# Optimization experiments

Hardware: AMD Instinct MI355X
Metric: run time of the kernel (lower is better)

The kernel has to match this reference:

```python
import math
import jax, jax.numpy as jnp
import numpy as np

D_MODEL, STATE_DIM, SEQ_L = 256, 64, 8192


def setup_inputs() -> dict:
    key = jax.random.key(0)
    ks = jax.random.split(key, 6)
    d, N = D_MODEL, STATE_DIM
    s = 1.0 / math.sqrt(N)
    return {
        "Lambda_re": jax.random.normal(ks[0], (d, N), jnp.float32),
        "Lambda_im": jax.random.normal(ks[1], (d, N), jnp.float32),
        "P_re": jax.random.normal(ks[2], (d, N), jnp.float32) * s,
        "P_im": jax.random.normal(ks[3], (d, N), jnp.float32) * s,
        "B_re": jax.random.normal(ks[4], (d, N), jnp.float32) * s,
        "B_im": jnp.zeros((d, N), jnp.float32),
        "log_dt": jax.random.uniform(ks[5], (d,), jnp.float32,
                                     math.log(1e-3), math.log(0.1)),
        "D": jnp.zeros((d,), jnpp := jnp.float32) if False else jnp.zeros((d,), jnp.float32),
        "L": SEQ_L,
    }


def reference(Lambda_re, Lambda_im, P_re, P_im, B_re, B_im, log_dt, D, L):
    # NPLR / Cauchy-Woodbury S4 kernel (learn_cd=False -> C = B, D is a zero buffer)
    Lam = (-jax.nn.softplus(Lambda_re) + 1j * Lambda_im).astype(jnp.complex64)  # [d, N]
    P = (P_re + 1j * P_im).astype(jnp.complex64)                                # [d, N]
    B = (B_re + 1j * B_im).astype(jnp.complex64)                                # [d, N]
    dt = jnp.exp(log_dt)                                                        # [d]

    k = jnp.arange(L)
    z = jnp.exp((-2j * jnp.pi / L) * k).astype(jnp.complex64)                   # [L] roots of unity
    eps = jnp.finfo(jnp.float32).eps
    denom_z = 1.0 + z
    denom_z = jnp.where(jnp.abs(denom_z) < eps, jnp.complex64(eps), denom_z)

    # Bilinear-transform frequencies g: [d, L] complex
    g = (2.0 / dt)[:, None] * ((1.0 - z) / denom_z)[None, :]

    # Cauchy resolvent R: [d, L, N] complex (the dominant intermediate)
    R = 1.0 / (g[:, :, None] - Lam[:, None, :])

    Pc, Bc = jnp.conj(P), jnp.conj(B)
    PRB = jnp.einsum('dn,dln,dn->dl', Pc, R, B)
    PRP = jnp.einsum('dn,dln,dn->dl', Pc, R, P)
    BRB = jnp.einsum('dn,dln,dn->dl', Bc, R, B)
    BRP = jnp.einsum('dn,dln,dn->dl', Bc, R, P)

    # Woodbury rank-1 correction, then undo the bilinear prefactor
    K_hat = (2.0 / denom_z)[None, :] * (BRB - BRP * PRB / (1.0 + PRP))          # [d, L]
    K = jnp.fft.ifft(K_hat, n=L, axis=-1).real.astype(jnp.float32)
    return (K, D)
```

## Files before the change

### kernel.cpp

```cpp
#include <hip/hip_runtime.h>
#include <math.h>

#ifndef M_PI
#define M_PI 3.14159265358979323846
#endif

#define DMODEL 256
#define NSTATE 64
#define LSEQ   8192
#define INVL   (1.0f/8192.0f)

#define OFF_TW  0
#define OFF_DN  (6144*8)
#define OFF_CDT (OFF_DN + DMODEL*NSTATE*32)

__device__ __forceinline__ float sin_rev(float r) {
#if __has_builtin(__builtin_amdgcn_sinf)
  return __builtin_amdgcn_sinf(r);
#else
  return __sinf(r * 6.283185307179586f);
#endif
}
__device__ __forceinline__ float cos_rev(float r) {
#if __has_builtin(__builtin_amdgcn_cosf)
  return __builtin_amdgcn_cosf(r);
#else
  return __cosf(r * 6.283185307179586f);
#endif
}

__device__ __forceinline__ float2 cmul(float2 a, float2 b) {
  return make_float2(a.x*b.x - a.y*b.y, a.x*b.y + a.y*b.x);
}

__device__ __forceinline__ float2 woodbury(float2 S1, float2 S2, float2 S3,
                                           float2 S4, float T) {
  float nr = (S1.x*S1.x - S1.y*S1.y) + (S2.x*S2.x - S2.y*S2.y);
  float ni = 2.0f*(S1.x*S1.y + S2.x*S2.y);
  float dr = 1.0f + S3.x, di = S3.y;
  float inv = __builtin_amdgcn_rcpf(fmaf(dr, dr, di*di));
  float qr = (nr*dr + ni*di) * inv;
  float qi = (ni*dr - nr*di) * inv;
  float vr = S4.x - qr, vi = S4.y - qi;
  return make_float2((vr - T*vi)*INVL, (vi + T*vr)*INVL);
}

__global__ __launch_bounds__(256) void precompute_kernel(
    const float* __restrict__ Lre, const float* __restrict__ Lim,
    const float* __restrict__ Pre, const float* __restrict__ Pim,
    const float* __restrict__ Bre, const float* __restrict__ Bim,
    const float* __restrict__ log_dt, char* __restrict__ ws)
{
  const int t = blockIdx.x * blockDim.x + threadIdx.x;
  float2* tw  = (float2*)(ws + OFF_TW);
  float4* dn  = (float4*)(ws + OFF_DN);
  float*  cdt = (float*)(ws + OFF_CDT);

  if (t < 6144) {
    double th = (2.0 * M_PI / (double)LSEQ) * (double)t;
    double s, c; sincos(th, &s, &c);
    tw[t] = make_float2((float)c, (float)s);
  }
  {
    float lre = Lre[t], lim = Lim[t];
    float pre = Pre[t], pim = Pim[t];
    float bre = Bre[t], bim = Bim[t];
    float sp = fmaxf(lre, 0.0f) + log1pf(expf(-fabsf(lre)));
    float w1r = pre*bre + pim*bim;
    float w1i = pre*bim - pim*bre;
    float w2  = pre*pre + pim*pim;
    float w3  = bre*bre + bim*bim;
    dn[2*t]   = make_float4(lim, sp, sp*sp, w1r);
    dn[2*t+1] = make_float4(w1i, w2, w3, 0.0f);
  }
  if (t < DMODEL) cdt[t] = 2.0f * expf(-log_dt[t]);
}

__global__ __launch_bounds__(1024) void fused_kernel(
    const float4* __restrict__ dn_all, const float* __restrict__ cdt,
    const float2* __restrict__ tw, const float* __restrict__ Din,
    float* __restrict__ out)
{
  __shared__ __align__(16) float2 xy[LSEQ];
  const int d = blockIdx.x;
  const int t = threadIdx.x;
  const float4* dn = dn_all + (size_t)d * (2*NSTATE);
  const float c = cdt[d];

  for (int it = 0; it < 4; ++it) {
    const int b = t + (it << 10);
    const unsigned p = (unsigned)(2*b);
    const unsigned r = __brev(p) >> 19;
    const int kA = (int)((r & 0x1000u) | ((r & 0x0555u) << 1) | ((r & 0x0AAAu) >> 1));
    const float rev = (float)kA * (1.0f/16384.0f);
    const float sA = sin_rev(rev), cAc = cos_rev(rev);
    float TA = sA * __builtin_amdgcn_rcpf(cAc);
    float TB = -cAc * __builtin_amdgcn_rcpf(sA);
    TA = fminf(fmaxf(TA, -1e7f), 1e7f);
    TB = fminf(fmaxf(TB, -1e7f), 1e7f);
    const float gA = c * TA, gB = c * TB;

    float2 S1a = {0,0}, S2a = {0,0}, S3a = {0,0}, S4a = {0,0};
    float2 S1b = {0,0}, S2b = {0,0}, S3b = {0,0}, S4b = {0,0};
#pragma unroll 8
    for (int n = 0; n < NSTATE; ++n) {
      const float4 a = dn[2*n];
      const float4 w = dn[2*n+1];
      {
        const float dim = gA - a.x;
        const float inv = __builtin_amdgcn_rcpf(fmaf(dim, dim, a.z));
        const float rr = a.y * inv;
        const float di = dim * inv;
        S1a.x = fmaf(a.w, rr, S1a.x);  S1a.y = fmaf(a.w, -di, S1a.y);
        S2a.x = fmaf(w.x, rr, S2a.x);  S2a.y = fmaf(w.x, -di, S2a.y);
        S3a.x = fmaf(w.y, rr, S3a.x);  S3a.y = fmaf(w.y, -di, S3a.y);
        S4a.x = fmaf(w.z, rr, S4a.x);  S4a.y = fmaf(w.z, -di, S4a.y);
      }
      {
        const float dim = gB - a.x;
        const float inv = __builtin_amdgcn_rcpf(fmaf(dim, dim, a.z));
        const float rr = a.y * inv;
        const float di = dim * inv;
        S1b.x = fmaf(a.w, rr, S1b.x);  S1b.y = fmaf(a.w, -di, S1b.y);
        S2b.x = fmaf(w.x, rr, S2b.x);  S2b.y = fmaf(w.x, -di, S2b.y);
        S3b.x = fmaf(w.y, rr, S3b.x);  S3b.y = fmaf(w.y, -di, S3b.y);
        S4b.x = fmaf(w.z, rr, S4b.x);  S4b.y = fmaf(w.z, -di, S4b.y);
      }
    }
    const float2 KA = woodbury(S1a, S2a, S3a, S4a, TA);
    const float2 KB = woodbury(S1b, S2b, S3b, S4b, TB);
    ((float4*)xy)[b] = make_float4(KA.x + KB.x, KA.y + KB.y,
                                   KA.x - KB.x, KA.y - KB.y);
  }
  __syncthreads();

#pragma unroll
  for (int s = 0; s < 6; ++s) {
    const int h = 2 << (2*s);
    const int twsh = 10 - 2*s;
#pragma unroll
    for (int j = 0; j < 2; ++j) {
      const int bb = t + (j << 10);
      const int pos = bb & (h - 1);
      const int i0 = ((bb >> (1 + 2*s)) << (3 + 2*s)) + pos;
      const int ti = pos << twsh;
      const float2 w1 = tw[ti];
      const float2 w2 = tw[2*ti];
      const float2 w3 = tw[3*ti];
      const float2 x0 = xy[i0];
      const float2 x1 = xy[i0 + h];
      const float2 x2 = xy[i0 + 2*h];
      const float2 x3 = xy[i0 + 3*h];
      const float2 t1 = cmul(w1, x1);
      const float2 t2 = cmul(w2, x2);
      const float2 t3 = cmul(w3, x3);
      const float2 u0 = make_float2(x0.x + t2.x, x0.y + t2.y);
      const float2 u1 = make_float2(x0.x - t2.x, x0.y - t2.y);
      const float2 u2 = make_float2(t1.x + t3.x, t1.y + t3.y);
      const float2 vv = make_float2(t1.x - t3.x, t1.y - t3.y);
      xy[i0]         = make_float2(u0.x + u2.x, u0.y + u2.y);
      xy[i0 + h]     = make_float2(u1.x - vv.y, u1.y + vv.x);
      xy[i0 + 2*h]   = make_float2(u0.x - u2.x, u0.y - u2.y);
      xy[i0 + 3*h]   = make_float2(u1.x + vv.y, u1.y - vv.x);
    }
    __syncthreads();
  }

  float* orow = out + (size_t)d * LSEQ;
  for (int i = t; i < LSEQ; i += 1024) orow[i] = xy[i].x;

  if (d == 0 && t < DMODEL) out[(size_t)DMODEL * LSEQ + t] = Din[t];
}

extern "C" void kernel_launch(void* const* d_in, const int* in_sizes, int n_in,
                              void* d_out, int out_size, void* d_ws, size_t ws_size,
                              hipStream_t stream)
{
  const float* Lre    = (const float*)d_in[0];
  const float* Lim    = (const float*)d_in[1];
  const float* Pre    = (const float*)d_in[2];
  const float* Pim    = (const float*)d_in[3];
  const float* Bre    = (const float*)d_in[4];
  const float* Bim    = (const float*)d_in[5];
  const float* log_dt = (const float*)d_in[6];
  const float* Din    = (const float*)d_in[7];
  float* out = (float*)d_out;
  char* ws = (char*)d_ws;

  hipLaunchKernelGGL(precompute_kernel, dim3(64), dim3(256), 0, stream,
                     Lre, Lim, Pre, Pim, Bre, Bim, log_dt, ws);
  hipLaunchKernelGGL(fused_kernel, dim3(DMODEL), dim3(1024), 0, stream,
                     (const float4*)(ws + OFF_DN), (const float*)(ws + OFF_CDT),
                     (const float2*)(ws + OFF_TW), Din, out);
}
```

Before: 123.9 us.

## Split fused kernel into parallel Cauchy kernel and separate iFFT kernel

```diff
diff --git a/kernel.cpp b/kernel.cpp
--- a/kernel.cpp
+++ b/kernel.cpp
@@ -12,7 +12,8 @@
 
 #define OFF_TW  0
 #define OFF_DN  (6144*8)
-#define OFF_CDT (OFF_DN + DMODEL*NSTATE*32)
+#define OFF_CDT (OFF_DN + DMODEL*NSTATE*48)
+#define OFF_KT  (OFF_CDT + 1024)
 
 __device__ __forceinline__ float sin_rev(float r) {
 #if __has_builtin(__builtin_amdgcn_sinf)
@@ -70,68 +71,75 @@
     float w1i = pre*bim - pim*bre;
     float w2  = pre*pre + pim*pim;
     float w3  = bre*bre + bim*bim;
-    dn[2*t]   = make_float4(lim, sp, sp*sp, w1r);
-    dn[2*t+1] = make_float4(w1i, w2, w3, 0.0f);
+    dn[3*t]   = make_float4(lim, sp*sp, w1r*sp, w1i*sp);
+    dn[3*t+1] = make_float4(w2*sp, w3*sp, w1r, w1i);
+    dn[3*t+2] = make_float4(w2, w3, 0.0f, 0.0f);
   }
   if (t < DMODEL) cdt[t] = 2.0f * expf(-log_dt[t]);
 }
 
-__global__ __launch_bounds__(1024) void fused_kernel(
+__global__ __launch_bounds__(256, 8) void cauchy_kernel(
     const float4* __restrict__ dn_all, const float* __restrict__ cdt,
-    const float2* __restrict__ tw, const float* __restrict__ Din,
-    float* __restrict__ out)
+    float4* __restrict__ kt)
+{
+  const int d = blockIdx.y;
+  const int b = blockIdx.x * 256 + threadIdx.x;
+  const float4* dn = dn_all + (size_t)d * (3*NSTATE);
+  const float c = cdt[d];
+
+  const unsigned p = (unsigned)(2*b);
+  const unsigned r = __brev(p) >> 19;
+  const int kA = (int)(((r & 0x0555u) << 1) | ((r & 0x0AAAu) >> 1));
+  const float rev = (float)kA * (1.0f/16384.0f);
+  const float sA = sin_rev(rev), cA = cos_rev(rev);
+  float TA = sA * __builtin_amdgcn_rcpf(cA);
+  float TB = -cA * __builtin_amdgcn_rcpf(sA);
+  TA = fminf(fmaxf(TA, -1e7f), 1e7f);
+  TB = fminf(fmaxf(TB, -1e7f), 1e7f);
+  const float gA = c * TA, gB = c * TB;
+
+  float2 S1a = {0,0}, S2a = {0,0}, S3a = {0,0}, S4a = {0,0};
+  float2 S1b = {0,0}, S2b = {0,0}, S3b = {0,0}, S4b = {0,0};
+#pragma unroll 4
+  for (int n = 0; n < NSTATE; ++n) {
+    const float4 q0 = dn[3*n];
+    const float4 q1 = dn[3*n+1];
+    const float4 q2 = dn[3*n+2];
+    {
+      const float dim = gA - q0.x;
+      const float inv = __builtin_amdgcn_rcpf(fmaf(dim, dim, q0.y));
+      const float dI  = dim * inv;
+      S1a.x = fmaf(q0.z, inv, S1a.x);  S1a.y = fmaf(q1.z, -dI, S1a.y);
+      S2a.x = fmaf(q0.w, inv, S2a.x);  S2a.y = fmaf(q1.w, -dI, S2a.y);
+      S3a.x = fmaf(q1.x, inv, S3a.x);  S3a.y = fmaf(q2.x, -dI, S3a.y);
+      S4a.x = fmaf(q1.y, inv, S4a.x);  S4a.y = fmaf(q2.y, -dI, S4a.y);
+    }
+    {
+      const float dim = gB - q0.x;
+      const float inv = __builtin_amdgcn_rcpf(fmaf(dim, dim, q0.y));
+      const float dI  = dim * inv;
+      S1b.x = fmaf(q0.z, inv, S1b.x);  S1b.y = fmaf(q1.z, -dI, S1b.y);
+      S2b.x = fmaf(q0.w, inv, S2b.x);  S2b.y = fmaf(q1.w, -dI, S2b.y);
+      S3b.x = fmaf(q1.x, inv, S3b.x);  S3b.y = fmaf(q2.x, -dI, S3b.y);
+      S4b.x = fmaf(q1.y, inv, S4b.x);  S4b.y = fmaf(q2.y, -dI, S4b.y);
+    }
+  }
+  const float2 KA = woodbury(S1a, S2a, S3a, S4a, TA);
+  const float2 KB = woodbury(S1b, S2b, S3b, S4b, TB);
+  kt[(size_t)d * 4096 + b] = make_float4(KA.x + KB.x, KA.y + KB.y,
+                                         KA.x - KB.x, KA.y - KB.y);
+}
+
+__global__ __launch_bounds__(1024) void ifft_kernel(
+    const float4* __restrict__ kt, const float2* __restrict__ tw,
+    const float* __restrict__ Din, float* __restrict__ out)
 {
   __shared__ __align__(16) float2 xy[LSEQ];
   const int d = blockIdx.x;
   const int t = threadIdx.x;
-  const float4* dn = dn_all + (size_t)d * (2*NSTATE);
-  const float c = cdt[d];
-
-  for (int it = 0; it < 4; ++it) {
-    const int b = t + (it << 10);
-    const unsigned p = (unsigned)(2*b);
-    const unsigned r = __brev(p) >> 19;
-    const int kA = (int)((r & 0x1000u) | ((r & 0x0555u) << 1) | ((r & 0x0AAAu) >> 1));
-    const float rev = (float)kA * (1.0f/16384.0f);
-    const float sA = sin_rev(rev), cAc = cos_rev(rev);
-    float TA = sA * __builtin_amdgcn_rcpf(cAc);
-    float TB = -cAc * __builtin_amdgcn_rcpf(sA);
-    TA = fminf(fmaxf(TA, -1e7f), 1e7f);
-    TB = fminf(fmaxf(TB, -1e7f), 1e7f);
-    const float gA = c * TA, gB = c * TB;
-
-    float2 S1a = {0,0}, S2a = {0,0}, S3a = {0,0}, S4a = {0,0};
-    float2 S1b = {0,0}, S2b = {0,0}, S3b = {0,0}, S4b = {0,0};
-#pragma unroll 8
-    for (int n = 0; n < NSTATE; ++n) {
-      const float4 a = dn[2*n];
-      const float4 w = dn[2*n+1];
-      {
-        const float dim = gA - a.x;
-        const float inv = __builtin_amdgcn_rcpf(fmaf(dim, dim, a.z));
-        const float rr = a.y * inv;
-        const float di = dim * inv;
-        S1a.x = fmaf(a.w, rr, S1a.x);  S1a.y = fmaf(a.w, -di, S1a.y);
-        S2a.x = fmaf(w.x, rr, S2a.x);  S2a.y = fmaf(w.x, -di, S2a.y);
-        S3a.x = fmaf(w.y, rr, S3a.x);  S3a.y = fmaf(w.y, -di, S3a.y);
-        S4a.x = fmaf(w.z, rr, S4a.x);  S4a.y = fmaf(w.z, -di, S4a.y);
-      }
-      {
-        const float dim = gB - a.x;
-        const float inv = __builtin_amdgcn_rcpf(fmaf(dim, dim, a.z));
-        const float rr = a.y * inv;
-        const float di = dim * inv;
-        S1b.x = fmaf(a.w, rr, S1b.x);  S1b.y = fmaf(a.w, -di, S1b.y);
-        S2b.x = fmaf(w.x, rr, S2b.x);  S2b.y = fmaf(w.x, -di, S2b.y);
-        S3b.x = fmaf(w.y, rr, S3b.x);  S3b.y = fmaf(w.y, -di, S3b.y);
-        S4b.x = fmaf(w.z, rr, S4b.x);  S4b.y = fmaf(w.z, -di, S4b.y);
-      }
-    }
-    const float2 KA = woodbury(S1a, S2a, S3a, S4a, TA);
-    const float2 KB = woodbury(S1b, S2b, S3b, S4b, TB);
-    ((float4*)xy)[b] = make_float4(KA.x + KB.x, KA.y + KB.y,
-                                   KA.x - KB.x, KA.y - KB.y);
-  }
+  const float4* row = kt + (size_t)d * 4096;
+
+  for (int i = t; i < 4096; i += 1024) ((float4*)xy)[i] = row[i];
   __syncthreads();
 
 #pragma unroll
@@ -189,7 +197,10 @@
 
   hipLaunchKernelGGL(precompute_kernel, dim3(64), dim3(256), 0, stream,
                      Lre, Lim, Pre, Pim, Bre, Bim, log_dt, ws);
-  hipLaunchKernelGGL(fused_kernel, dim3(DMODEL), dim3(1024), 0, stream,
+  hipLaunchKernelGGL(cauchy_kernel, dim3(16, DMODEL), dim3(256), 0, stream,
                      (const float4*)(ws + OFF_DN), (const float*)(ws + OFF_CDT),
-                     (const float2*)(ws + OFF_TW), Din, out);
-}
+                     (float4*)(ws + OFF_KT));
+  hipLaunchKernelGGL(ifft_kernel, dim3(DMODEL), dim3(1024), 0, stream,
+                     (const float4*)(ws + OFF_KT), (const float2*)(ws + OFF_TW),
+                     Din, out);
+}
```

Result: slower. 129.9 us (+4.8%).
